# Kernel tuning notes

Hardware: AMD Instinct MI355X
Metric: run time of the kernel (lower is better)

The kernel has to match this reference:

```python
import jax, jax.numpy as jnp
import numpy as np
import math

D_MODEL = 128
N_HEADS = 4
DIM_FF = 256
B, L = 4, 2048
EPS = 1e-5
NEG = -1e9


def _layernorm(x, g, b):
    mu = jnp.mean(x, axis=-1, keepdims=True)
    var = jnp.mean((x - mu) ** 2, axis=-1, keepdims=True)
    return (x - mu) * jax.lax.rsqrt(var + EPS) * g + b


def setup_inputs() -> dict:
    key = jax.random.key(0)
    ks = jax.random.split(key, 16)
    s = 1.0 / math.sqrt(D_MODEL)
    return {
        "h": jax.random.normal(ks[0], (B, L, D_MODEL), jnp.float32),
        "attn_bias": jax.random.normal(ks[1], (B, N_HEADS, L, L), jnp.float32),
        "node_mask": jax.random.randint(ks[2], (B, L), 0, 2).astype(jnp.float32),
        "sparse_mask": jax.random.randint(ks[3], (B, L, L), 0, 2).astype(bool),
        "w_qkv": jax.random.normal(ks[4], (3 * D_MODEL, D_MODEL), jnp.float32) * s,
        "b_qkv": jnp.zeros((3 * D_MODEL,), jnp.float32),
        "w_out": jax.random.normal(ks[5], (D_MODEL, D_MODEL), jnp.float32) * s,
        "b_out": jnp.zeros((D_MODEL,), jnp.float32),
        "w_ff1": jax.random.normal(ks[6], (DIM_FF, D_MODEL), jnp.float32) * s,
        "b_ff1": jnp.zeros((DIM_FF,), jnp.float32),
        "w_ff2": jax.random.normal(ks[7], (D_MODEL, DIM_FF), jnp.float32) * (1.0 / math.sqrt(DIM_FF)),
        "b_ff2": jnp.zeros((D_MODEL,), jnp.float32),
        "ln1_g": jnp.ones((D_MODEL,), jnp.float32),
        "ln1_b": jnp.zeros((D_MODEL,), jnp.float32),
        "ln2_g": jnp.ones((D_MODEL,), jnp.float32),
        "ln2_b": jnp.zeros((D_MODEL,), jnp.float32),
    }


def reference(h, attn_bias, node_mask, sparse_mask, w_qkv, b_qkv, w_out, b_out,
              w_ff1, b_ff1, w_ff2, b_ff2, ln1_g, ln1_b, ln2_g, ln2_b):
    bsz, lsz, dsz = h.shape
    dk = dsz // N_HEADS
    qkv = h @ w_qkv.T + b_qkv  # [B,L,3D]
    q, k, v = jnp.split(qkv, 3, axis=-1)
    # [B,L,D] -> [B,H,L,dk]
    q = q.reshape(bsz, lsz, N_HEADS, dk).transpose(0, 2, 1, 3)
    k = k.reshape(bsz, lsz, N_HEADS, dk).transpose(0, 2, 1, 3)
    v = v.reshape(bsz, lsz, N_HEADS, dk).transpose(0, 2, 1, 3)
    scores = jnp.einsum("bhqd,bhkd->bhqk", q, k) / math.sqrt(dk)
    scores = scores + attn_bias
    scores = jnp.where(sparse_mask[:, None, :, :], scores, NEG)
    key_mask = node_mask[:, None, None, :] > 0
    scores = jnp.where(key_mask, scores, NEG)
    attn = jax.nn.softmax(scores, axis=-1)
    attn = attn * (node_mask[:, None, :, None] > 0).astype(attn.dtype)
    out = jnp.einsum("bhqk,bhkd->bhqd", attn, v)
    out = out.transpose(0, 2, 1, 3).reshape(bsz, lsz, dsz)
    out = out @ w_out.T + b_out
    h1 = _layernorm(h + out, ln1_g, ln1_b)
    ff = jax.nn.relu(h1 @ w_ff1.T + b_ff1) @ w_ff2.T + b_ff2
    h2 = _layernorm(h1 + ff, ln2_g, ln2_b)
    return h2 * node_mask[:, :, None]
```

## Files before the change

kernel.cpp:

```cpp
#include <hip/hip_runtime.h>
#include <math.h>

#define NEG_INF (-1e9f)
#define EPS 1e-5f

typedef __attribute__((ext_vector_type(8))) short short8;
typedef __attribute__((ext_vector_type(4))) float floatx4;

__device__ __forceinline__ unsigned short f2bf(float x) {
    union { float f; unsigned u; } v; v.f = x;
    unsigned r = v.u + 0x7fffu + ((v.u >> 16) & 1u);
    return (unsigned short)(r >> 16);
}

__device__ __forceinline__ void gl2lds16(const void* g, void* l) {
    __builtin_amdgcn_global_load_lds(
        (const __attribute__((address_space(1))) unsigned int*)g,
        (__attribute__((address_space(3))) unsigned int*)l, 16, 0, 0);
}

__global__ void transpose_prep_kernel(const float* __restrict__ w_qkv, const float* __restrict__ w_out,
                                      const float* __restrict__ w_ff1, const float* __restrict__ w_ff2,
                                      float* __restrict__ wqkvT, float* __restrict__ woutT,
                                      float* __restrict__ wff1T, float* __restrict__ wff2T,
                                      const unsigned int* __restrict__ sm, int* __restrict__ flag,
                                      const float* __restrict__ nm, unsigned int* __restrict__ nmb) {
    if (blockIdx.x < 512) {
        int idx = blockIdx.x * 256 + threadIdx.x;
        if (idx < 49152) {
            int r = idx / 128, c = idx % 128;
            wqkvT[c * 384 + r] = w_qkv[idx];
        } else if (idx < 65536) {
            int i = idx - 49152; int r = i / 128, c = i % 128;
            woutT[c * 128 + r] = w_out[i];
        } else if (idx < 98304) {
            int i = idx - 65536; int r = i / 128, c = i % 128;
            wff1T[c * 256 + r] = w_ff1[i];
        } else {
            int i = idx - 98304; int r = i / 256, c = i % 256;
            wff2T[c * 128 + r] = w_ff2[i];
        }
    } else if (blockIdx.x == 512) {
        __shared__ int bad;
        if (threadIdx.x == 0) bad = 0;
        __syncthreads();
        for (int i = threadIdx.x; i < 4096; i += 256) {
            if (sm[i] > 1u) bad = 1;
        }
        __syncthreads();
        if (threadIdx.x == 0) *flag = bad;
    } else {
        const int t = threadIdx.x;
        const int b = t >> 6, w32 = t & 63;
        unsigned u = 0;
#pragma unroll
        for (int j = 0; j < 32; ++j)
            u |= (nm[b * 2048 + w32 * 32 + j] > 0.f ? 1u : 0u) << j;
        nmb[t] = u;
    }
}

__global__ void mask_prep_kernel(const unsigned char* __restrict__ smraw,
                                 const int* __restrict__ flag,
                                 const unsigned int* __restrict__ nmb,
                                 unsigned int* __restrict__ cbits) {
    const int idx = blockIdx.x * 256 + threadIdx.x;
    const int b = idx >> 17;
    const int q = (idx >> 6) & 2047;
    const int w32 = idx & 63;
    unsigned u = 0;
    if (*flag) {
        const uint4* p = reinterpret_cast<const uint4*>(
            smraw + (size_t)(b * 2048 + q) * 2048 + w32 * 32);
        uint4 a = p[0], c = p[1];
        unsigned wd0 = a.x, wd1 = a.y, wd2 = a.z, wd3 = a.w;
        unsigned wd4 = c.x, wd5 = c.y, wd6 = c.z, wd7 = c.w;
#define BYTES4(v, sh) \
        u |= ((v) & 0xffu ? 1u : 0u) << (sh); \
        u |= ((v) & 0xff00u ? 1u : 0u) << ((sh) + 1); \
        u |= ((v) & 0xff0000u ? 1u : 0u) << ((sh) + 2); \
        u |= ((v) & 0xff000000u ? 1u : 0u) << ((sh) + 3);
        BYTES4(wd0, 0) BYTES4(wd1, 4) BYTES4(wd2, 8) BYTES4(wd3, 12)
        BYTES4(wd4, 16) BYTES4(wd5, 20) BYTES4(wd6, 24) BYTES4(wd7, 28)
#undef BYTES4
    } else {
        const uint4* p = reinterpret_cast<const uint4*>(
            reinterpret_cast<const unsigned int*>(smraw) + (size_t)(b * 2048 + q) * 2048 + w32 * 32);
#pragma unroll
        for (int wi = 0; wi < 8; ++wi) {
            uint4 a = p[wi];
            u |= (a.x ? 1u : 0u) << (wi * 4);
            u |= (a.y ? 1u : 0u) << (wi * 4 + 1);
            u |= (a.z ? 1u : 0u) << (wi * 4 + 2);
            u |= (a.w ? 1u : 0u) << (wi * 4 + 3);
        }
    }
    cbits[idx] = u & nmb[b * 64 + w32];
}

__global__ void qkv_kernel(const float* __restrict__ h, const float* __restrict__ wT,
                           const float* __restrict__ bqkv,
                           unsigned short* __restrict__ qb, unsigned short* __restrict__ kbm,
                           unsigned short* __restrict__ vtb) {
    __shared__ __align__(16) float hs[16 * 128];
    const int tid = threadIdx.x;
    const int row0 = blockIdx.x * 16;
    for (int i = tid; i < 2048; i += 384) hs[i] = h[row0 * 128 + i];
    __syncthreads();

    const int c = tid;
    float acc[16];
#pragma unroll
    for (int r = 0; r < 16; ++r) acc[r] = 0.f;

    for (int d0 = 0; d0 < 128; d0 += 4) {
        float w0 = wT[(d0 + 0) * 384 + c];
        float w1 = wT[(d0 + 1) * 384 + c];
        float w2 = wT[(d0 + 2) * 384 + c];
        float w3 = wT[(d0 + 3) * 384 + c];
#pragma unroll
        for (int r = 0; r < 16; ++r) {
            float4 h4 = *reinterpret_cast<const float4*>(&hs[r * 128 + d0]);
            acc[r] = fmaf(w0, h4.x, acc[r]);
            acc[r] = fmaf(w1, h4.y, acc[r]);
            acc[r] = fmaf(w2, h4.z, acc[r]);
            acc[r] = fmaf(w3, h4.w, acc[r]);
        }
    }
    const int part = c >> 7;
    const int cc = c & 127;
    const int head = cc >> 5;
    const int dd = cc & 31;
    const float bias = bqkv[c];
    const float scale = (part == 0) ? 0.17677669529663687f : 1.0f;
#pragma unroll
    for (int r = 0; r < 16; ++r) {
        int grow = row0 + r;
        int b = grow >> 11, l = grow & 2047;
        int bh = b * 4 + head;
        unsigned short val = f2bf((acc[r] + bias) * scale);
        if (part == 0)      qb[((size_t)bh * 2048 + l) * 32 + dd] = val;
        else if (part == 1) kbm[((size_t)bh * 2048 + l) * 32 + dd] = val;
        else                vtb[((size_t)bh * 32 + dd) * 2048 + l] = val;
    }
}

__global__ __launch_bounds__(256, 2) void attn_kernel(
        const unsigned short* __restrict__ qb, const unsigned short* __restrict__ kbm,
        const unsigned short* __restrict__ vtb, const float* __restrict__ bias,
        const unsigned int* __restrict__ cbits, const float* __restrict__ nmask,
        float* __restrict__ aout) {
    __shared__ __align__(16) unsigned short k_lds[128 * 32];
    __shared__ __align__(16) unsigned short v_lds[32 * 128];
    __shared__ __align__(16) float bias_lds[2][32 * 128];
    __shared__ __align__(16) unsigned short p_lds[4][16 * 72];
    __shared__ float merge_lds[2][64][10];

    const int tid = threadIdx.x;
    const int w = tid >> 6, L = tid & 63;
    const int qsub = w & 1, khalf = w >> 1;
    const int lb = (blockIdx.x & 7) * 128 + (blockIdx.x >> 3);
    const int bh = lb >> 6, qt = lb & 63;
    const int b = bh >> 2, hh = bh & 3;
    const int q0b = qt * 32;
    const int q = L & 15, g = L >> 4;

    const unsigned short* kb_g = kbm + (size_t)bh * 2048 * 32;
    const unsigned short* vb_g = vtb + (size_t)bh * 32 * 2048;
    const float* bias_q0 = bias + ((size_t)bh * 2048 + q0b) * 2048;
    const short8 qf = *reinterpret_cast<const short8*>(
        qb + ((size_t)bh * 2048 + q0b + qsub * 16 + q) * 32 + g * 8);
    const unsigned int* crow = cbits + (size_t)(b * 2048 + q0b + qsub * 16 + q) * 64 + khalf * 2;

    const int kcsrc = (tid & 3) ^ ((tid >> 2) & 3);
    const int vcsrc = (tid & 15) ^ (tid >> 4);
    const int brow0 = tid >> 5;

    auto stage_kv = [&](int kt) {
        const int k0 = kt * 128;
#pragma unroll
        for (int i = 0; i < 2; ++i) {
            int row = i * 64 + (tid >> 2);
            gl2lds16(kb_g + (size_t)(k0 + row) * 32 + kcsrc * 8,
                     (char*)k_lds + i * 4096 + w * 1024);
        }
#pragma unroll
        for (int i = 0; i < 2; ++i) {
            int row = i * 16 + (tid >> 4);
            gl2lds16(vb_g + (size_t)row * 2048 + k0 + vcsrc * 8,
                     (char*)v_lds + i * 4096 + w * 1024);
        }
    };
    auto stage_bias = [&](int buf, int kt) {
        const int k0 = kt * 128;
#pragma unroll
        for (int i = 0; i < 4; ++i) {
            int row = i * 8 + brow0;
            int csrc = (tid & 31) ^ ((i & 1) * 8 + brow0) ^ ((brow0 & 1) << 4);
            gl2lds16(bias_q0 + (size_t)row * 2048 + k0 + csrc * 4,
                     (char*)(&bias_lds[buf][0]) + i * 4096 + w * 1024);
        }
    };

    stage_kv(0);
    stage_bias(0, 0);
    stage_bias(1, 1);
    asm volatile("s_waitcnt vmcnt(4)" ::: "memory");
    __builtin_amdgcn_s_barrier();

    float mrun = -3.0e38f, lrun = 0.f;
    floatx4 o0 = {0.f, 0.f, 0.f, 0.f}, o1 = {0.f, 0.f, 0.f, 0.f};
    const floatx4 zacc = {0.f, 0.f, 0.f, 0.f};
    unsigned short* pl = &p_lds[w][q * 72];

    const char* klbase = (const char*)k_lds + (khalf * 64 + q) * 64 + ((g ^ (q & 3)) << 4);
    const int vo0 = q * 256 + (((khalf * 8 + g) ^ q) << 4);
    const int vo1 = q * 256 + (((khalf * 8 + 4 + g) ^ q) << 4);
    const int R = qsub * 16 + q;
    const int bswz = q ^ ((q & 1) << 4);
    int boff[4];
#pragma unroll
    for (int mm = 0; mm < 4; ++mm)
        boff[mm] = R * 512 + (((khalf * 16 + 4 * mm + g) ^ bswz) << 4);

    for (int t = 0; t < 16; ++t) {
        const int cur = t & 1;

        short8 kf0 = *reinterpret_cast<const short8*>(klbase + 0 * 1024);
        short8 kf1 = *reinterpret_cast<const short8*>(klbase + 1 * 1024);
        short8 kf2 = *reinterpret_cast<const short8*>(klbase + 2 * 1024);
        short8 kf3 = *reinterpret_cast<const short8*>(klbase + 3 * 1024);
        const char* vl = (const char*)v_lds;
        short8 vf00 = *reinterpret_cast<const short8*>(vl + vo0);
        short8 vf01 = *reinterpret_cast<const short8*>(vl + vo1);
        short8 vf10 = *reinterpret_cast<const short8*>(vl + 4096 + vo0);
        short8 vf11 = *reinterpret_cast<const short8*>(vl + 4096 + vo1);
        uint2 cw = *reinterpret_cast<const uint2*>(crow + t * 4);

        float s[16];
        {
            floatx4 r0 = __builtin_amdgcn_mfma_f32_16x16x32_bf16(kf0, qf, zacc, 0, 0, 0);
            floatx4 r1 = __builtin_amdgcn_mfma_f32_16x16x32_bf16(kf1, qf, zacc, 0, 0, 0);
            floatx4 r2 = __builtin_amdgcn_mfma_f32_16x16x32_bf16(kf2, qf, zacc, 0, 0, 0);
            floatx4 r3 = __builtin_amdgcn_mfma_f32_16x16x32_bf16(kf3, qf, zacc, 0, 0, 0);
            s[0] = r0[0]; s[1] = r0[1]; s[2] = r0[2]; s[3] = r0[3];
            s[4] = r1[0]; s[5] = r1[1]; s[6] = r1[2]; s[7] = r1[3];
            s[8] = r2[0]; s[9] = r2[1]; s[10] = r2[2]; s[11] = r2[3];
            s[12] = r3[0]; s[13] = r3[1]; s[14] = r3[2]; s[15] = r3[3];
        }
        const char* bl = (const char*)(&bias_lds[cur][0]);
        float4 bq0 = *reinterpret_cast<const float4*>(bl + boff[0]);
        float4 bq1 = *reinterpret_cast<const float4*>(bl + boff[1]);
        float4 bq2 = *reinterpret_cast<const float4*>(bl + boff[2]);
        float4 bq3 = *reinterpret_cast<const float4*>(bl + boff[3]);
        float bvv[16];
        bvv[0] = bq0.x; bvv[1] = bq0.y; bvv[2] = bq0.z; bvv[3] = bq0.w;
        bvv[4] = bq1.x; bvv[5] = bq1.y; bvv[6] = bq1.z; bvv[7] = bq1.w;
        bvv[8] = bq2.x; bvv[9] = bq2.y; bvv[10] = bq2.z; bvv[11] = bq2.w;
        bvv[12] = bq3.x; bvv[13] = bq3.y; bvv[14] = bq3.z; bvv[15] = bq3.w;
#pragma unroll
        for (int i = 0; i < 16; ++i) {
            const int mm = i >> 2, reg = i & 3;
            const unsigned word = (mm < 2) ? cw.x : cw.y;
            const int sh = 16 * (mm & 1) + 4 * g + reg;
            const bool keep = (word >> sh) & 1;
            s[i] = keep ? (s[i] + bvv[i]) : NEG_INF;
        }
        float tm = s[0];
#pragma unroll
        for (int i = 1; i < 16; ++i) tm = fmaxf(tm, s[i]);
        tm = fmaxf(tm, __shfl_xor(tm, 16));
        tm = fmaxf(tm, __shfl_xor(tm, 32));
        const float mn = fmaxf(mrun, tm);
        const float f = __expf(mrun - mn);
        mrun = mn;
        float p[16], ts = 0.f;
#pragma unroll
        for (int i = 0; i < 16; ++i) { p[i] = __expf(s[i] - mn); ts += p[i]; }
        ts += __shfl_xor(ts, 16);
        ts += __shfl_xor(ts, 32);
        lrun = lrun * f + ts;
        o0 *= f; o1 *= f;
#pragma unroll
        for (int mm = 0; mm < 4; ++mm) {
            unsigned u0 = (unsigned)f2bf(p[4 * mm]) | ((unsigned)f2bf(p[4 * mm + 1]) << 16);
            unsigned u1 = (unsigned)f2bf(p[4 * mm + 2]) | ((unsigned)f2bf(p[4 * mm + 3]) << 16);
            *reinterpret_cast<unsigned int*>(pl + 16 * mm + 4 * g) = u0;
            *reinterpret_cast<unsigned int*>(pl + 16 * mm + 4 * g + 2) = u1;
        }
        short8 pb0 = *reinterpret_cast<const short8*>(pl + g * 8);
        short8 pb1 = *reinterpret_cast<const short8*>(pl + 32 + g * 8);
        o0 = __builtin_amdgcn_mfma_f32_16x16x32_bf16(vf00, pb0, o0, 0, 0, 0);
        o0 = __builtin_amdgcn_mfma_f32_16x16x32_bf16(vf01, pb1, o0, 0, 0, 0);
        o1 = __builtin_amdgcn_mfma_f32_16x16x32_bf16(vf10, pb0, o1, 0, 0, 0);
        o1 = __builtin_amdgcn_mfma_f32_16x16x32_bf16(vf11, pb1, o1, 0, 0, 0);

        if (t < 15) {
            __builtin_amdgcn_s_barrier();
            stage_kv(t + 1);
            if (t + 2 < 16) {
                stage_bias(cur, t + 2);
                asm volatile("s_waitcnt vmcnt(4)" ::: "memory");
            } else {
                asm volatile("s_waitcnt vmcnt(0)" ::: "memory");
            }
            __builtin_amdgcn_s_barrier();
        }
    }

    if (khalf == 1) {
        float* dst = merge_lds[qsub][L];
        dst[0] = mrun; dst[1] = lrun;
        dst[2] = o0[0]; dst[3] = o0[1]; dst[4] = o0[2]; dst[5] = o0[3];
        dst[6] = o1[0]; dst[7] = o1[1]; dst[8] = o1[2]; dst[9] = o1[3];
    }
    __syncthreads();
    if (khalf == 0) {
        const float* src = merge_lds[qsub][L];
        const float m2 = src[0], l2 = src[1];
        const float mm = fmaxf(mrun, m2);
        const float f1 = __expf(mrun - mm), f2 = __expf(m2 - mm);
        const float l = lrun * f1 + l2 * f2;
        const int qrow = q0b + qsub * 16 + q;
        const float nmq = nmask[b * 2048 + qrow];
        const float inv = (nmq > 0.f) ? (1.f / l) : 0.f;
        const float a1 = f1 * inv, a2 = f2 * inv;
        float* op = aout + ((size_t)b * 2048 + qrow) * 128 + hh * 32 + g * 4;
        *reinterpret_cast<float4*>(op) = make_float4(
            o0[0] * a1 + src[2] * a2, o0[1] * a1 + src[3] * a2,
            o0[2] * a1 + src[4] * a2, o0[3] * a1 + src[5] * a2);
        *reinterpret_cast<float4*>(op + 16) = make_float4(
            o1[0] * a1 + src[6] * a2, o1[1] * a1 + src[7] * a2,
            o1[2] * a1 + src[8] * a2, o1[3] * a1 + src[9] * a2);
    }
}

__device__ __forceinline__ void ln_stats(const float* buf, float* mu_s, float* rs_s, int tid) {
    int row = tid >> 4, sl = tid & 15;
    float4 x0 = *reinterpret_cast<const float4*>(&buf[row * 128 + sl * 8]);
    float4 x1 = *reinterpret_cast<const float4*>(&buf[row * 128 + sl * 8 + 4]);
    float sum = x0.x + x0.y + x0.z + x0.w + x1.x + x1.y + x1.z + x1.w;
    float sq = x0.x * x0.x + x0.y * x0.y + x0.z * x0.z + x0.w * x0.w +
               x1.x * x1.x + x1.y * x1.y + x1.z * x1.z + x1.w * x1.w;
#pragma unroll
    for (int off = 8; off > 0; off >>= 1) {
        sum += __shfl_xor(sum, off);
        sq += __shfl_xor(sq, off);
    }
    if (sl == 0) {
        float mu = sum * (1.f / 128.f);
        float var = sq * (1.f / 128.f) - mu * mu;
        mu_s[row] = mu;
        rs_s[row] = rsqrtf(var + EPS);
    }
}

__global__ void epilogue_kernel(const float* __restrict__ aout, const float* __restrict__ h,
                                const float* __restrict__ woutT, const float* __restrict__ bout,
                                const float* __restrict__ wff1T, const float* __restrict__ bff1,
                                const float* __restrict__ wff2T, const float* __restrict__ bff2,
                                const float* __restrict__ g1, const float* __restrict__ b1,
                                const float* __restrict__ g2, const float* __restrict__ b2,
                                const float* __restrict__ nmask, float* __restrict__ out) {
    __shared__ __align__(16) float A[16 * 128];
    __shared__ __align__(16) float Hb[16 * 128];
    __shared__ __align__(16) float F[16 * 256];
    __shared__ float mu_s[16], rs_s[16];

    const int tid = threadIdx.x;
    const int row0 = blockIdx.x * 16;
    for (int i = tid; i < 2048; i += 256) {
        A[i] = aout[row0 * 128 + i];
        Hb[i] = h[row0 * 128 + i];
    }
    __syncthreads();

    const int g = tid >> 7, c = tid & 127;

    float acc[8];
#pragma unroll
    for (int r = 0; r < 8; ++r) acc[r] = 0.f;
    for (int d0 = 0; d0 < 128; d0 += 4) {
        float w0 = woutT[(d0 + 0) * 128 + c];
        float w1 = woutT[(d0 + 1) * 128 + c];
        float w2 = woutT[(d0 + 2) * 128 + c];
        float w3 = woutT[(d0 + 3) * 128 + c];
#pragma unroll
        for (int r = 0; r < 8; ++r) {
            float4 a4 = *reinterpret_cast<const float4*>(&A[(g * 8 + r) * 128 + d0]);
            acc[r] = fmaf(w0, a4.x, acc[r]);
            acc[r] = fmaf(w1, a4.y, acc[r]);
            acc[r] = fmaf(w2, a4.z, acc[r]);
            acc[r] = fmaf(w3, a4.w, acc[r]);
        }
    }
    float bo = bout[c];
#pragma unroll
    for (int r = 0; r < 8; ++r) {
        int row = g * 8 + r;
        Hb[row * 128 + c] += acc[r] + bo;
    }
    __syncthreads();

    ln_stats(Hb, mu_s, rs_s, tid);
    __syncthreads();
    float g1c = g1[c], b1c = b1[c];
#pragma unroll
    for (int r = 0; r < 8; ++r) {
        int row = g * 8 + r;
        float v = (Hb[row * 128 + c] - mu_s[row]) * rs_s[row] * g1c + b1c;
        Hb[row * 128 + c] = v;
    }
    __syncthreads();

    {
        const int j = tid;
        float a2[16];
#pragma unroll
        for (int r = 0; r < 16; ++r) a2[r] = 0.f;
        for (int d0 = 0; d0 < 128; d0 += 4) {
            float w0 = wff1T[(d0 + 0) * 256 + j];
            float w1 = wff1T[(d0 + 1) * 256 + j];
            float w2 = wff1T[(d0 + 2) * 256 + j];
            float w3 = wff1T[(d0 + 3) * 256 + j];
#pragma unroll
            for (int r = 0; r < 16; ++r) {
                float4 h4 = *reinterpret_cast<const float4*>(&Hb[r * 128 + d0]);
                a2[r] = fmaf(w0, h4.x, a2[r]);
                a2[r] = fmaf(w1, h4.y, a2[r]);
                a2[r] = fmaf(w2, h4.z, a2[r]);
                a2[r] = fmaf(w3, h4.w, a2[r]);
            }
        }
        float bj = bff1[j];
#pragma unroll
        for (int r = 0; r < 16; ++r) F[r * 256 + j] = fmaxf(a2[r] + bj, 0.f);
    }
    __syncthreads();

    float a3[8];
#pragma unroll
    for (int r = 0; r < 8; ++r) a3[r] = 0.f;
    for (int d0 = 0; d0 < 256; d0 += 4) {
        float w0 = wff2T[(d0 + 0) * 128 + c];
        float w1 = wff2T[(d0 + 1) * 128 + c];
        float w2 = wff2T[(d0 + 2) * 128 + c];
        float w3 = wff2T[(d0 + 3) * 128 + c];
#pragma unroll
        for (int r = 0; r < 8; ++r) {
            float4 f4 = *reinterpret_cast<const float4*>(&F[(g * 8 + r) * 256 + d0]);
            a3[r] = fmaf(w0, f4.x, a3[r]);
            a3[r] = fmaf(w1, f4.y, a3[r]);
            a3[r] = fmaf(w2, f4.z, a3[r]);
            a3[r] = fmaf(w3, f4.w, a3[r]);
        }
    }
    float bo2 = bff2[c];
#pragma unroll
    for (int r = 0; r < 8; ++r) {
        int row = g * 8 + r;
        A[row * 128 + c] = a3[r] + bo2 + Hb[row * 128 + c];
    }
    __syncthreads();

    ln_stats(A, mu_s, rs_s, tid);
    __syncthreads();
    float g2c = g2[c], b2c = b2[c];
#pragma unroll
    for (int r = 0; r < 8; ++r) {
        int row = g * 8 + r;
        float nm = nmask[row0 + row];
        float v = (A[row * 128 + c] - mu_s[row]) * rs_s[row] * g2c + b2c;
        out[(row0 + row) * 128 + c] = v * nm;
    }
}

extern "C" void kernel_launch(void* const* d_in, const int* in_sizes, int n_in,
                              void* d_out, int out_size, void* d_ws, size_t ws_size,
                              hipStream_t stream) {
    const float* h = (const float*)d_in[0];
    const float* bias = (const float*)d_in[1];
    const float* nmask = (const float*)d_in[2];
    const void* smask = d_in[3];
    const float* w_qkv = (const float*)d_in[4];
    const float* b_qkv = (const float*)d_in[5];
    const float* w_out = (const float*)d_in[6];
    const float* b_out = (const float*)d_in[7];
    const float* w_ff1 = (const float*)d_in[8];
    const float* b_ff1 = (const float*)d_in[9];
    const float* w_ff2 = (const float*)d_in[10];
    const float* b_ff2 = (const float*)d_in[11];
    const float* g1 = (const float*)d_in[12];
    const float* b1 = (const float*)d_in[13];
    const float* g2 = (const float*)d_in[14];
    const float* b2 = (const float*)d_in[15];
    float* out = (float*)d_out;

    char* wsb = (char*)d_ws;
    float* aoutw = (float*)wsb;
    unsigned short* qb  = (unsigned short*)(wsb + (4 << 20));
    unsigned short* kbm = (unsigned short*)(wsb + (6 << 20));
    unsigned short* vtb = (unsigned short*)(wsb + (8 << 20));
    unsigned int* cbits = (unsigned int*)(wsb + (10 << 20));
    unsigned int* nmb   = (unsigned int*)(wsb + (12 << 20));
    float* wqkvT = (float*)(wsb + (12 << 20) + 4096);
    float* woutT = wqkvT + 384 * 128;
    float* wff1T = woutT + 128 * 128;
    float* wff2T = wff1T + 256 * 128;
    int* smflag = (int*)(wff2T + 128 * 256);

    transpose_prep_kernel<<<514, 256, 0, stream>>>(w_qkv, w_out, w_ff1, w_ff2,
                                                   wqkvT, woutT, wff1T, wff2T,
                                                   (const unsigned int*)smask, smflag,
                                                   nmask, nmb);
    mask_prep_kernel<<<2048, 256, 0, stream>>>((const unsigned char*)smask, smflag, nmb, cbits);
    qkv_kernel<<<512, 384, 0, stream>>>(h, wqkvT, b_qkv, qb, kbm, vtb);
    attn_kernel<<<1024, 256, 0, stream>>>(qb, kbm, vtb, bias, cbits, nmask, aoutw);
    epilogue_kernel<<<512, 256, 0, stream>>>(aoutw, h, woutT, b_out, wff1T, b_ff1,
                                             wff2T, b_ff2, g1, b1, g2, b2, nmask, out);
}
```

Measured before the change: 163.8 us.

## Halve attention key tile to 64 and deepen K/V and bias prefetch pipeline

The attention loop now walks 64-key tiles over 32 iterations instead of 128-key tiles over 16. K/V are double-buffered two tiles ahead, and attn_bias is quad-buffered three tiles ahead. The LDS swizzles and fragment offsets are redone for the smaller tiles. The goal is to hide the latency of the large bias stream behind more in-flight loads, at the cost of twice as many barrier pairs per block and less MFMA work per iteration. At the tail, redundant clamped loads of the last tile are issued.

```diff
diff --git a/kernel.cpp b/kernel.cpp
--- a/kernel.cpp
+++ b/kernel.cpp
@@ -150,10 +150,10 @@
         const unsigned short* __restrict__ vtb, const float* __restrict__ bias,
         const unsigned int* __restrict__ cbits, const float* __restrict__ nmask,
         float* __restrict__ aout) {
-    __shared__ __align__(16) unsigned short k_lds[128 * 32];
-    __shared__ __align__(16) unsigned short v_lds[32 * 128];
-    __shared__ __align__(16) float bias_lds[2][32 * 128];
-    __shared__ __align__(16) unsigned short p_lds[4][16 * 72];
+    __shared__ __align__(16) unsigned short k_lds[2][64 * 32];
+    __shared__ __align__(16) unsigned short v_lds[2][32 * 64];
+    __shared__ __align__(16) float bias_lds[4][32 * 64];
+    __shared__ __align__(16) unsigned short p_lds[4][16 * 40];
     __shared__ float merge_lds[2][64][10];
 
     const int tid = threadIdx.x;
@@ -170,140 +170,121 @@
     const float* bias_q0 = bias + ((size_t)bh * 2048 + q0b) * 2048;
     const short8 qf = *reinterpret_cast<const short8*>(
         qb + ((size_t)bh * 2048 + q0b + qsub * 16 + q) * 32 + g * 8);
-    const unsigned int* crow = cbits + (size_t)(b * 2048 + q0b + qsub * 16 + q) * 64 + khalf * 2;
-
-    const int kcsrc = (tid & 3) ^ ((tid >> 2) & 3);
-    const int vcsrc = (tid & 15) ^ (tid >> 4);
-    const int brow0 = tid >> 5;
-
-    auto stage_kv = [&](int kt) {
-        const int k0 = kt * 128;
-#pragma unroll
-        for (int i = 0; i < 2; ++i) {
-            int row = i * 64 + (tid >> 2);
-            gl2lds16(kb_g + (size_t)(k0 + row) * 32 + kcsrc * 8,
-                     (char*)k_lds + i * 4096 + w * 1024);
-        }
+    const unsigned int* crow = cbits + (size_t)(b * 2048 + q0b + qsub * 16 + q) * 64;
+
+    const int krow = tid >> 2, kc = tid & 3;
+    const int kf_st = (krow & 3) ^ ((krow >> 2) & 3);
+    const int vrow = tid >> 3, vc = tid & 7;
+
+    auto stage_kv = [&](int buf, int kt) {
+        const int k0 = kt * 64;
+        gl2lds16(kb_g + (size_t)(k0 + krow) * 32 + ((kc ^ kf_st) << 3),
+                 (char*)(&k_lds[buf][0]) + w * 1024);
+        gl2lds16(vb_g + (size_t)vrow * 2048 + k0 + ((vc ^ (vrow & 7)) << 3),
+                 (char*)(&v_lds[buf][0]) + w * 1024);
+    };
+    auto stage_bias = [&](int buf, int kt) {
+        const int k0 = kt * 64;
 #pragma unroll
         for (int i = 0; i < 2; ++i) {
             int row = i * 16 + (tid >> 4);
-            gl2lds16(vb_g + (size_t)row * 2048 + k0 + vcsrc * 8,
-                     (char*)v_lds + i * 4096 + w * 1024);
+            int csrc = (tid & 15) ^ (row & 7);
+            gl2lds16(bias_q0 + (size_t)row * 2048 + k0 + (csrc << 2),
+                     (char*)(&bias_lds[buf][0]) + i * 4096 + w * 1024);
         }
     };
-    auto stage_bias = [&](int buf, int kt) {
-        const int k0 = kt * 128;
-#pragma unroll
-        for (int i = 0; i < 4; ++i) {
-            int row = i * 8 + brow0;
-            int csrc = (tid & 31) ^ ((i & 1) * 8 + brow0) ^ ((brow0 & 1) << 4);
-            gl2lds16(bias_q0 + (size_t)row * 2048 + k0 + csrc * 4,
-                     (char*)(&bias_lds[buf][0]) + i * 4096 + w * 1024);
-        }
-    };
-
-    stage_kv(0);
+
+    stage_kv(0, 0);
     stage_bias(0, 0);
+    stage_kv(1, 1);
     stage_bias(1, 1);
-    asm volatile("s_waitcnt vmcnt(4)" ::: "memory");
+    stage_bias(2, 2);
+    asm volatile("s_waitcnt vmcnt(6)" ::: "memory");
     __builtin_amdgcn_s_barrier();
 
     float mrun = -3.0e38f, lrun = 0.f;
     floatx4 o0 = {0.f, 0.f, 0.f, 0.f}, o1 = {0.f, 0.f, 0.f, 0.f};
     const floatx4 zacc = {0.f, 0.f, 0.f, 0.f};
-    unsigned short* pl = &p_lds[w][q * 72];
-
-    const char* klbase = (const char*)k_lds + (khalf * 64 + q) * 64 + ((g ^ (q & 3)) << 4);
-    const int vo0 = q * 256 + (((khalf * 8 + g) ^ q) << 4);
-    const int vo1 = q * 256 + (((khalf * 8 + 4 + g) ^ q) << 4);
+    unsigned short* pl = &p_lds[w][q * 40];
+
+    const int r0k = khalf * 32 + q;
+    const int fk = (q & 3) ^ ((q >> 2) & 3);
+    const int koff0 = r0k * 64 + ((g ^ fk) << 4);
+    const int koff1 = (r0k + 16) * 64 + ((g ^ fk) << 4);
+    const int vch = khalf * 4 + g;
+    const int voff0 = q * 128 + ((vch ^ (q & 7)) << 4);
+    const int voff1 = (16 + q) * 128 + ((vch ^ (q & 7)) << 4);
     const int R = qsub * 16 + q;
-    const int bswz = q ^ ((q & 1) << 4);
-    int boff[4];
-#pragma unroll
-    for (int mm = 0; mm < 4; ++mm)
-        boff[mm] = R * 512 + (((khalf * 16 + 4 * mm + g) ^ bswz) << 4);
-
-    for (int t = 0; t < 16; ++t) {
+    const int j0 = khalf * 8 + g;
+    const int boff0 = R * 256 + (((j0    ) ^ (R & 7)) << 4);
+    const int boff1 = R * 256 + (((j0 + 4) ^ (R & 7)) << 4);
+
+    for (int t = 0; t < 32; ++t) {
         const int cur = t & 1;
-
-        short8 kf0 = *reinterpret_cast<const short8*>(klbase + 0 * 1024);
-        short8 kf1 = *reinterpret_cast<const short8*>(klbase + 1 * 1024);
-        short8 kf2 = *reinterpret_cast<const short8*>(klbase + 2 * 1024);
-        short8 kf3 = *reinterpret_cast<const short8*>(klbase + 3 * 1024);
-        const char* vl = (const char*)v_lds;
-        short8 vf00 = *reinterpret_cast<const short8*>(vl + vo0);
-        short8 vf01 = *reinterpret_cast<const short8*>(vl + vo1);
-        short8 vf10 = *reinterpret_cast<const short8*>(vl + 4096 + vo0);
-        short8 vf11 = *reinterpret_cast<const short8*>(vl + 4096 + vo1);
-        uint2 cw = *reinterpret_cast<const uint2*>(crow + t * 4);
-
-        float s[16];
-        {
-            floatx4 r0 = __builtin_amdgcn_mfma_f32_16x16x32_bf16(kf0, qf, zacc, 0, 0, 0);
-            floatx4 r1 = __builtin_amdgcn_mfma_f32_16x16x32_bf16(kf1, qf, zacc, 0, 0, 0);
-            floatx4 r2 = __builtin_amdgcn_mfma_f32_16x16x32_bf16(kf2, qf, zacc, 0, 0, 0);
-            floatx4 r3 = __builtin_amdgcn_mfma_f32_16x16x32_bf16(kf3, qf, zacc, 0, 0, 0);
-            s[0] = r0[0]; s[1] = r0[1]; s[2] = r0[2]; s[3] = r0[3];
-            s[4] = r1[0]; s[5] = r1[1]; s[6] = r1[2]; s[7] = r1[3];
-            s[8] = r2[0]; s[9] = r2[1]; s[10] = r2[2]; s[11] = r2[3];
-            s[12] = r3[0]; s[13] = r3[1]; s[14] = r3[2]; s[15] = r3[3];
-        }
-        const char* bl = (const char*)(&bias_lds[cur][0]);
-        float4 bq0 = *reinterpret_cast<const float4*>(bl + boff[0]);
-        float4 bq1 = *reinterpret_cast<const float4*>(bl + boff[1]);
-        float4 bq2 = *reinterpret_cast<const float4*>(bl + boff[2]);
-        float4 bq3 = *reinterpret_cast<const float4*>(bl + boff[3]);
-        float bvv[16];
+        const int bcur = t & 3;
+
+        const char* kl = (const char*)(&k_lds[cur][0]);
+        short8 kf0 = *reinterpret_cast<const short8*>(kl + koff0);
+        short8 kf1 = *reinterpret_cast<const short8*>(kl + koff1);
+        const char* vl = (const char*)(&v_lds[cur][0]);
+        short8 vf0 = *reinterpret_cast<const short8*>(vl + voff0);
+        short8 vf1 = *reinterpret_cast<const short8*>(vl + voff1);
+        const char* bl = (const char*)(&bias_lds[bcur][0]);
+        float4 bq0 = *reinterpret_cast<const float4*>(bl + boff0);
+        float4 bq1 = *reinterpret_cast<const float4*>(bl + boff1);
+        const unsigned cw = crow[2 * t + khalf];
+
+        floatx4 rr0 = __builtin_amdgcn_mfma_f32_16x16x32_bf16(kf0, qf, zacc, 0, 0, 0);
+        floatx4 rr1 = __builtin_amdgcn_mfma_f32_16x16x32_bf16(kf1, qf, zacc, 0, 0, 0);
+        float s[8];
+        s[0] = rr0[0]; s[1] = rr0[1]; s[2] = rr0[2]; s[3] = rr0[3];
+        s[4] = rr1[0]; s[5] = rr1[1]; s[6] = rr1[2]; s[7] = rr1[3];
+        float bvv[8];
         bvv[0] = bq0.x; bvv[1] = bq0.y; bvv[2] = bq0.z; bvv[3] = bq0.w;
         bvv[4] = bq1.x; bvv[5] = bq1.y; bvv[6] = bq1.z; bvv[7] = bq1.w;
-        bvv[8] = bq2.x; bvv[9] = bq2.y; bvv[10] = bq2.z; bvv[11] = bq2.w;
-        bvv[12] = bq3.x; bvv[13] = bq3.y; bvv[14] = bq3.z; bvv[15] = bq3.w;
-#pragma unroll
-        for (int i = 0; i < 16; ++i) {
+#pragma unroll
+        for (int i = 0; i < 8; ++i) {
             const int mm = i >> 2, reg = i & 3;
-            const unsigned word = (mm < 2) ? cw.x : cw.y;
-            const int sh = 16 * (mm & 1) + 4 * g + reg;
-            const bool keep = (word >> sh) & 1;
+            const int sh = mm * 16 + 4 * g + reg;
+            const bool keep = (cw >> sh) & 1;
             s[i] = keep ? (s[i] + bvv[i]) : NEG_INF;
         }
         float tm = s[0];
 #pragma unroll
-        for (int i = 1; i < 16; ++i) tm = fmaxf(tm, s[i]);
+        for (int i = 1; i < 8; ++i) tm = fmaxf(tm, s[i]);
         tm = fmaxf(tm, __shfl_xor(tm, 16));
         tm = fmaxf(tm, __shfl_xor(tm, 32));
         const float mn = fmaxf(mrun, tm);
         const float f = __expf(mrun - mn);
         mrun = mn;
-        float p[16], ts = 0.f;
-#pragma unroll
-        for (int i = 0; i < 16; ++i) { p[i] = __expf(s[i] - mn); ts += p[i]; }
+        float p[8], ts = 0.f;
+#pragma unroll
+        for (int i = 0; i < 8; ++i) { p[i] = __expf(s[i] - mn); ts += p[i]; }
         ts += __shfl_xor(ts, 16);
         ts += __shfl_xor(ts, 32);
         lrun = lrun * f + ts;
         o0 *= f; o1 *= f;
-#pragma unroll
-        for (int mm = 0; mm < 4; ++mm) {
-            unsigned u0 = (unsigned)f2bf(p[4 * mm]) | ((unsigned)f2bf(p[4 * mm + 1]) << 16);
-            unsigned u1 = (unsigned)f2bf(p[4 * mm + 2]) | ((unsigned)f2bf(p[4 * mm + 3]) << 16);
-            *reinterpret_cast<unsigned int*>(pl + 16 * mm + 4 * g) = u0;
-            *reinterpret_cast<unsigned int*>(pl + 16 * mm + 4 * g + 2) = u1;
-        }
-        short8 pb0 = *reinterpret_cast<const short8*>(pl + g * 8);
-        short8 pb1 = *reinterpret_cast<const short8*>(pl + 32 + g * 8);
-        o0 = __builtin_amdgcn_mfma_f32_16x16x32_bf16(vf00, pb0, o0, 0, 0, 0);
-        o0 = __builtin_amdgcn_mfma_f32_16x16x32_bf16(vf01, pb1, o0, 0, 0, 0);
-        o1 = __builtin_amdgcn_mfma_f32_16x16x32_bf16(vf10, pb0, o1, 0, 0, 0);
-        o1 = __builtin_amdgcn_mfma_f32_16x16x32_bf16(vf11, pb1, o1, 0, 0, 0);
-
-        if (t < 15) {
+        {
+            unsigned u0 = (unsigned)f2bf(p[0]) | ((unsigned)f2bf(p[1]) << 16);
+            unsigned u1 = (unsigned)f2bf(p[2]) | ((unsigned)f2bf(p[3]) << 16);
+            unsigned u2 = (unsigned)f2bf(p[4]) | ((unsigned)f2bf(p[5]) << 16);
+            unsigned u3 = (unsigned)f2bf(p[6]) | ((unsigned)f2bf(p[7]) << 16);
+            *reinterpret_cast<unsigned int*>(pl + 4 * g) = u0;
+            *reinterpret_cast<unsigned int*>(pl + 4 * g + 2) = u1;
+            *reinterpret_cast<unsigned int*>(pl + 16 + 4 * g) = u2;
+            *reinterpret_cast<unsigned int*>(pl + 16 + 4 * g + 2) = u3;
+        }
+        short8 pb = *reinterpret_cast<const short8*>(pl + 8 * g);
+        o0 = __builtin_amdgcn_mfma_f32_16x16x32_bf16(vf0, pb, o0, 0, 0, 0);
+        o1 = __builtin_amdgcn_mfma_f32_16x16x32_bf16(vf1, pb, o1, 0, 0, 0);
+
+        if (t < 31) {
             __builtin_amdgcn_s_barrier();
-            stage_kv(t + 1);
-            if (t + 2 < 16) {
-                stage_bias(cur, t + 2);
-                asm volatile("s_waitcnt vmcnt(4)" ::: "memory");
-            } else {
-                asm volatile("s_waitcnt vmcnt(0)" ::: "memory");
-            }
+            const int kt2 = (t + 2 > 31) ? 31 : t + 2;
+            const int bt3 = (t + 3 > 31) ? 31 : t + 3;
+            stage_kv(cur, kt2);
+            stage_bias((t + 3) & 3, bt3);
+            asm volatile("s_waitcnt vmcnt(6)" ::: "memory");
             __builtin_amdgcn_s_barrier();
         }
     }
```

Measured after the change: 181.2 us. 1.11x slower.
